# Performance work log

Measured on AMD Instinct MI355X. Metric: run time of the kernel, lower is better.

The kernel has to match this reference:

```python
import jax, jax.numpy as jnp
import numpy as np
import math

N_HEAD = 12

def _tiled_causal_mask(T):
    # t x t lower-triangular mask tiled 3x3 -> T x T (T divisible by 3)
    t = T // 3
    tril = jnp.tril(jnp.ones((t, t), dtype=bool))
    return jnp.tile(tril, (3, 3))  # [T, T]

def setup_inputs() -> dict:
    key = jax.random.key(0)
    ks = jax.random.split(key, 5)
    B, T, C = 4, 1536, 768
    s = 1.0 / math.sqrt(C)
    return {
        "x": jax.random.normal(ks[0], (B, T, C), dtype=jnp.float32),
        "Wq": jax.random.normal(ks[1], (C, C), dtype=jnp.float32) * s,
        "bq": jnp.zeros((C,), dtype=jnp.float32),
        "Wk": jax.random.normal(ks[2], (C, C), dtype=jnp.float32) * s,
        "bk": jnp.zeros((C,), dtype=jnp.float32),
        "Wv": jax.random.normal(ks[3], (C, C), dtype=jnp.float32) * s,
        "bv": jnp.zeros((C,), dtype=jnp.float32),
        "Wp": jax.random.normal(ks[4], (C, C), dtype=jnp.float32) * s,
        "bp": jnp.zeros((C,), dtype=jnp.float32),
    }

def reference(x, Wq, bq, Wk, bk, Wv, bv, Wp, bp):
    B, T, C = x.shape
    H = N_HEAD
    D = C // H  # head dim
    def heads(W, b):
        return (x @ W.T + b).reshape(B, T, H, D).transpose(0, 2, 1, 3)  # [B,H,T,D]
    q = heads(Wq, bq)
    k = heads(Wk, bk)
    v = heads(Wv, bv)
    att = jnp.einsum('bhqd,bhkd->bhqk', q, k) * (1.0 / math.sqrt(D))  # [B,H,T,T]
    mask = _tiled_causal_mask(T)  # [T,T] bool
    att = jnp.where(mask[None, None], att, jnp.float32(-jnp.inf))
    att = jax.nn.softmax(att, axis=-1)
    y = jnp.einsum('bhqk,bhkd->bhqd', att, v)  # [B,H,T,D]
    y = y.transpose(0, 2, 1, 3).reshape(B, T, C)
    return y @ Wp.T + bp
```

## Files before the change

### kernel.cpp

```cpp
#include <hip/hip_runtime.h>
#include <hip/hip_bf16.h>

typedef __attribute__((ext_vector_type(8))) short bf16x8;
typedef __attribute__((ext_vector_type(4))) float f32x4;

#define NH 12
#define HD 64
#define TT 1536
#define CC 768
#define BB 4
#define MM (BB * TT)
#define LOG2E 1.44269504088896f
#define SSHIFT 14.4269504089f

__device__ __forceinline__ unsigned short f2bf(float f) {
    unsigned int u = __builtin_bit_cast(unsigned int, f);
    return (unsigned short)((u + 0x7FFFu + ((u >> 16) & 1u)) >> 16);
}

__device__ __forceinline__ unsigned short nbf(float f) {
    __hip_bfloat16 h = __float2bfloat16(f);
    return __builtin_bit_cast(unsigned short, h);
}

__device__ __forceinline__ void gl_lds16(const unsigned short* g, unsigned short* l) {
    __builtin_amdgcn_global_load_lds(
        (const __attribute__((address_space(1))) void*)g,
        (__attribute__((address_space(3))) void*)l,
        16, 0, 0);
}

#define N4W (CC * CC / 4)
#define N4X (MM * CC / 4)
__global__ __launch_bounds__(256) void convert_all(
    const float* __restrict__ x,
    const float* __restrict__ w0, const float* __restrict__ w1,
    const float* __restrict__ w2, const float* __restrict__ w3,
    unsigned short* __restrict__ xo,
    unsigned short* __restrict__ o0, unsigned short* __restrict__ o1,
    unsigned short* __restrict__ o2, unsigned short* __restrict__ o3) {
    int i = blockIdx.x * 256 + threadIdx.x;
    const float* in;
    unsigned short* out;
    int j;
    if (i < N4X) {
        in = x; out = xo; j = i;
    } else {
        int t = i - N4X;
        int which = t / N4W;
        j = t - which * N4W;
        in = which == 0 ? w0 : which == 1 ? w1 : which == 2 ? w2 : w3;
        out = which == 0 ? o0 : which == 1 ? o1 : which == 2 ? o2 : o3;
    }
    float4 v = reinterpret_cast<const float4*>(in)[j];
    ushort4 o = { f2bf(v.x), f2bf(v.y), f2bf(v.z), f2bf(v.w) };
    reinterpret_cast<ushort4*>(out)[j] = o;
}

#define GEMM_KLOOP(APTR, BPTR)                                                \
    for (int kt = 0; kt < 12; kt++) {                                         \
        const int k0 = kt * 64;                                               \
        __syncthreads();                                                      \
        _Pragma("unroll")                                                     \
        for (int i = 0; i < 4; i++) {                                         \
            gl_lds16(&APTR[(size_t)(m0 + i * 32 + sr) * CC + k0 + sc],        \
                     as0 + (i * 32 + w * 8) * 64);                            \
            gl_lds16(&BPTR[(size_t)(n0 + i * 32 + sr) * CC + k0 + sc],        \
                     bs0 + (i * 32 + w * 8) * 64);                            \
        }                                                                     \
        __syncthreads();                                                      \
        _Pragma("unroll")                                                     \
        for (int s = 0; s < 2; s++) {                                         \
            const int swz = ((s * 4 + fg) ^ (fr & 7)) * 8;                    \
            bf16x8 a[4], b[4];                                                \
            _Pragma("unroll")                                                 \
            for (int mi = 0; mi < 4; mi++)                                    \
                a[mi] = *reinterpret_cast<const bf16x8*>(                     \
                    as0 + (wr * 64 + mi * 16 + fr) * 64 + swz);               \
            _Pragma("unroll")                                                 \
            for (int ni = 0; ni < 4; ni++)                                    \
                b[ni] = *reinterpret_cast<const bf16x8*>(                     \
                    bs0 + (wc * 64 + ni * 16 + fr) * 64 + swz);               \
            _Pragma("unroll")                                                 \
            for (int mi = 0; mi < 4; mi++)                                    \
                _Pragma("unroll")                                             \
                for (int ni = 0; ni < 4; ni++)                                \
                    acc[mi][ni] = __builtin_amdgcn_mfma_f32_16x16x32_bf16(    \
                        a[mi], b[ni], acc[mi][ni], 0, 0, 0);                  \
        }                                                                     \
    }

__global__ __launch_bounds__(256) void gemm_qkv(
    const unsigned short* __restrict__ xb,
    const unsigned short* __restrict__ wq, const float* __restrict__ bq,
    const unsigned short* __restrict__ wk, const float* __restrict__ bk,
    const unsigned short* __restrict__ wv, const float* __restrict__ bv,
    unsigned short* __restrict__ qo, unsigned short* __restrict__ ko,
    unsigned short* __restrict__ vo) {
    __shared__ unsigned short As[128][64];
    __shared__ unsigned short Bs[128][64];

    const int wg = (blockIdx.x & 7) * 108 + (blockIdx.x >> 3);
    const int z = wg / 288;
    const int rem = wg % 288;
    const int m0 = (rem / 6) * 128;
    const int n0 = (rem % 6) * 128;

    const unsigned short* W = (z == 0) ? wq : (z == 1) ? wk : wv;
    const float* bias = (z == 0) ? bq : (z == 1) ? bk : bv;
    unsigned short* out = (z == 0) ? qo : (z == 1) ? ko : vo;
    const float scale = (z == 0) ? 0.125f * LOG2E : 1.0f;

    const int tid = threadIdx.x;
    const int lane = tid & 63;
    const int w = tid >> 6;
    const int wr = w >> 1, wc = w & 1;
    const int fr = lane & 15, fg = lane >> 4;

    const int sr = tid >> 3;
    const int sc = ((tid & 7) ^ ((tid >> 3) & 7)) * 8;
    unsigned short* as0 = &As[0][0];
    unsigned short* bs0 = &Bs[0][0];

    f32x4 acc[4][4];
#pragma unroll
    for (int ni = 0; ni < 4; ni++) {
        float bv_ = bias[n0 + wc * 64 + ni * 16 + fr];
#pragma unroll
        for (int mi = 0; mi < 4; mi++)
            acc[mi][ni] = (f32x4){bv_, bv_, bv_, bv_};
    }

    GEMM_KLOOP(xb, W)

#pragma unroll
    for (int mi = 0; mi < 4; mi++)
#pragma unroll
        for (int ni = 0; ni < 4; ni++) {
            int n = n0 + wc * 64 + ni * 16 + fr;
            int h = n >> 6, d = n & 63;
            int m_base = m0 + wr * 64 + mi * 16 + fg * 4;
            int b_ = m_base / TT, t0 = m_base % TT;
            if (z == 2) {
                size_t off = ((size_t)(b_ * NH + h) * HD + d) * (size_t)TT + t0;
                ushort4 o = { nbf(acc[mi][ni][0]), nbf(acc[mi][ni][1]),
                              nbf(acc[mi][ni][2]), nbf(acc[mi][ni][3]) };
                *reinterpret_cast<ushort4*>(&out[off]) = o;
            } else {
#pragma unroll
                for (int r = 0; r < 4; r++) {
                    size_t off = ((size_t)(b_ * NH + h) * TT + t0 + r) * (size_t)HD + d;
                    out[off] = nbf(acc[mi][ni][r] * scale);
                }
            }
        }
}

__global__ __launch_bounds__(256) void gemm_proj(
    const unsigned short* __restrict__ yb,
    const unsigned short* __restrict__ wp, const float* __restrict__ bp,
    float* __restrict__ out) {
    __shared__ unsigned short As[128][64];
    __shared__ unsigned short Bs[128][64];

    const int wg = (blockIdx.x & 7) * 36 + (blockIdx.x >> 3);
    const int m0 = (wg / 6) * 128;
    const int n0 = (wg % 6) * 128;

    const int tid = threadIdx.x;
    const int lane = tid & 63;
    const int w = tid >> 6;
    const int wr = w >> 1, wc = w & 1;
    const int fr = lane & 15, fg = lane >> 4;

    const int sr = tid >> 3;
    const int sc = ((tid & 7) ^ ((tid >> 3) & 7)) * 8;
    unsigned short* as0 = &As[0][0];
    unsigned short* bs0 = &Bs[0][0];

    f32x4 acc[4][4];
#pragma unroll
    for (int ni = 0; ni < 4; ni++) {
        float bv_ = bp[n0 + wc * 64 + ni * 16 + fr];
#pragma unroll
        for (int mi = 0; mi < 4; mi++)
            acc[mi][ni] = (f32x4){bv_, bv_, bv_, bv_};
    }

    GEMM_KLOOP(yb, wp)

#pragma unroll
    for (int mi = 0; mi < 4; mi++)
#pragma unroll
        for (int ni = 0; ni < 4; ni++) {
            int n = n0 + wc * 64 + ni * 16 + fr;
#pragma unroll
            for (int r = 0; r < 4; r++) {
                int m = m0 + wr * 64 + mi * 16 + fg * 4 + r;
                out[(size_t)m * CC + n] = acc[mi][ni][r];
            }
        }
}

__global__ __launch_bounds__(256) void attn(
    const unsigned short* __restrict__ q, const unsigned short* __restrict__ k,
    const unsigned short* __restrict__ vt, unsigned short* __restrict__ y) {
    __shared__ unsigned short Ks[2][32][72];
    __shared__ unsigned short Vs[2][64][40];
    __shared__ unsigned short Ps[4][16][40];

    const int gid = blockIdx.x;
    const int slot = gid & 7;
    const int sub = (gid >> 3) % 6;
    const int bh = slot * 6 + sub;
    const int qt = gid / 48;
    const int qseg = 7 - qt / 3;
    const int sg0 = qt % 3;
    const int q0 = sg0 * 512 + qseg * 64;

    const int tid = threadIdx.x;
    const int w = tid >> 6;
    const int lane = tid & 63;
    const int fr = lane & 15, fg = lane >> 4;

    const size_t base = (size_t)bh * TT * HD;

    bf16x8 aq[2];
#pragma unroll
    for (int s = 0; s < 2; s++)
        aq[s] = *reinterpret_cast<const bf16x8*>(
            &q[base + (size_t)(q0 + w * 16 + fr) * HD + s * 32 + fg * 8]);

    f32x4 acc_o[4];
#pragma unroll
    for (int i = 0; i < 4; i++) acc_o[i] = (f32x4){0.f, 0.f, 0.f, 0.f};
    f32x4 acc_l = (f32x4){0.f, 0.f, 0.f, 0.f};

    const bf16x8 ones8 = {(short)0x3F80, (short)0x3F80, (short)0x3F80, (short)0x3F80,
                          (short)0x3F80, (short)0x3F80, (short)0x3F80, (short)0x3F80};
    const f32x4 sinit = {-SSHIFT, -SSHIFT, -SSHIFT, -SSHIFT};

    const int kr = tid >> 3, kc = tid & 7;
    const int vr = tid >> 2, vc = tid & 3;

    uint4 kreg, vreg;
    auto issue = [&](int k0n) {
        kreg = *reinterpret_cast<const uint4*>(&k[base + (size_t)(k0n + kr) * HD + kc * 8]);
        vreg = *reinterpret_cast<const uint4*>(&vt[base + (size_t)vr * TT + k0n + vc * 8]);
    };
    auto wlds = [&](int b) {
        *reinterpret_cast<uint4*>(&Ks[b][kr][kc * 8]) = kreg;
        *reinterpret_cast<uint4*>(&Vs[b][vr][vc * 8]) = vreg;
    };

    const int per = 2 * qseg + 2;
    const int ntot = 3 * per;

    issue(0);
    wlds(0);
    int cur = 0;
    int j = 0;
    int ji = 0, si = 0;

    for (int ci = 0; ci < ntot; ci++) {
        if (ci + 1 < ntot) {
            ji++; if (ji == per) { ji = 0; si++; }
            issue(si * 512 + ji * 32);
        }
        __syncthreads();

        f32x4 S[2];
#pragma unroll
        for (int nb = 0; nb < 2; nb++) {
            f32x4 sa = sinit;
#pragma unroll
            for (int s = 0; s < 2; s++) {
                bf16x8 bk_ = *reinterpret_cast<const bf16x8*>(
                    &Ks[cur][nb * 16 + fr][s * 32 + fg * 8]);
                sa = __builtin_amdgcn_mfma_f32_16x16x32_bf16(aq[s], bk_, sa, 0, 0, 0);
            }
            S[nb] = sa;
        }

        if (j >= 2 * qseg) {
            const int joff = (j - 2 * qseg) * 32;
#pragma unroll
            for (int nb = 0; nb < 2; nb++)
#pragma unroll
                for (int r = 0; r < 4; r++) {
                    int ib = w * 16 + fg * 4 + r;
                    int jb = joff + nb * 16 + fr;
                    if (jb > ib) S[nb][r] = -1e30f;
                }
        }

#pragma unroll
        for (int nb = 0; nb < 2; nb++)
#pragma unroll
            for (int r = 0; r < 4; r++)
                Ps[w][fg * 4 + r][((nb ^ (fg >> 1)) * 16) + fr] =
                    nbf(exp2f(S[nb][r]));

        bf16x8 ap = *reinterpret_cast<const bf16x8*>(
            &Ps[w][fr][(fg ^ (2 * (fr >> 3))) * 8]);
#pragma unroll
        for (int nd = 0; nd < 4; nd++) {
            bf16x8 bv_ = *reinterpret_cast<const bf16x8*>(&Vs[cur][nd * 16 + fr][fg * 8]);
            acc_o[nd] = __builtin_amdgcn_mfma_f32_16x16x32_bf16(ap, bv_, acc_o[nd], 0, 0, 0);
        }
        acc_l = __builtin_amdgcn_mfma_f32_16x16x32_bf16(ap, ones8, acc_l, 0, 0, 0);

        if (ci + 1 < ntot) wlds(cur ^ 1);
        cur ^= 1;
        if (++j == per) j = 0;
    }

    const int b_ = bh / NH, h = bh % NH;
#pragma unroll
    for (int r = 0; r < 4; r++) {
        float inv = 1.f / acc_l[r];
        int t = q0 + w * 16 + fg * 4 + r;
        size_t off = ((size_t)b_ * TT + t) * CC + h * HD;
#pragma unroll
        for (int nd = 0; nd < 4; nd++)
            y[off + nd * 16 + fr] = nbf(acc_o[nd][r] * inv);
    }
}

extern "C" void kernel_launch(void* const* d_in, const int* in_sizes, int n_in,
                              void* d_out, int out_size, void* d_ws, size_t ws_size,
                              hipStream_t stream) {
    const float* x  = (const float*)d_in[0];
    const float* Wq = (const float*)d_in[1];
    const float* bq = (const float*)d_in[2];
    const float* Wk = (const float*)d_in[3];
    const float* bk = (const float*)d_in[4];
    const float* Wv = (const float*)d_in[5];
    const float* bv = (const float*)d_in[6];
    const float* Wp = (const float*)d_in[7];
    const float* bp = (const float*)d_in[8];
    float* out = (float*)d_out;

    unsigned short* ws  = (unsigned short*)d_ws;
    unsigned short* wqb = ws;
    unsigned short* wkb = wqb + (size_t)CC * CC;
    unsigned short* wvb = wkb + (size_t)CC * CC;
    unsigned short* wpb = wvb + (size_t)CC * CC;
    unsigned short* xb  = wpb + (size_t)CC * CC;
    unsigned short* qb_ = xb  + (size_t)MM * CC;
    unsigned short* kb_ = qb_ + (size_t)MM * CC;
    unsigned short* vt_ = kb_ + (size_t)MM * CC;
    unsigned short* yb  = vt_ + (size_t)MM * CC;

    const int ntot4 = N4X + 4 * N4W;
    convert_all<<<(ntot4 + 255) / 256, 256, 0, stream>>>(
        x, Wq, Wk, Wv, Wp, xb, wqb, wkb, wvb, wpb);

    gemm_qkv<<<dim3(864), 256, 0, stream>>>(
        xb, wqb, bq, wkb, bk, wvb, bv, qb_, kb_, vt_);
    attn<<<dim3(48 * 24), 256, 0, stream>>>(qb_, kb_, vt_, yb);
    gemm_proj<<<dim3(288), 256, 0, stream>>>(yb, wpb, bp, out);
}
```

Baseline: 108.8 us.

## Shrink attention blocks to 32-row query tiles with XOR-swizzled LDS tiles

The attention kernel now runs two waves per block over 32 query rows instead of four waves over 64 rows, and launches twice as many blocks. The diagonal mask applies only to the last key tile of each segment, so fewer partially-masked tiles are processed. K and V shared-memory tiles drop their padding and use an XOR swizzle to avoid bank conflicts, with each thread loading two 16-byte chunks. The aim is finer causal load balancing, less wasted masked work, and less LDS. The cost is that each K/V tile is shared by fewer waves, so more global traffic per unit of compute.

```diff
diff --git a/kernel.cpp b/kernel.cpp
--- a/kernel.cpp
+++ b/kernel.cpp
@@ -202,21 +202,21 @@
         }
 }
 
-__global__ __launch_bounds__(256) void attn(
+__global__ __launch_bounds__(128) void attn(
     const unsigned short* __restrict__ q, const unsigned short* __restrict__ k,
     const unsigned short* __restrict__ vt, unsigned short* __restrict__ y) {
-    __shared__ unsigned short Ks[2][32][72];
-    __shared__ unsigned short Vs[2][64][40];
-    __shared__ unsigned short Ps[4][16][40];
+    __shared__ unsigned short Ks[2][32][64];
+    __shared__ unsigned short Vs[2][64][32];
+    __shared__ unsigned short Ps[2][16][40];
 
     const int gid = blockIdx.x;
     const int slot = gid & 7;
-    const int sub = (gid >> 3) % 6;
-    const int bh = slot * 6 + sub;
-    const int qt = gid / 48;
-    const int qseg = 7 - qt / 3;
-    const int sg0 = qt % 3;
-    const int q0 = sg0 * 512 + qseg * 64;
+    const int rest = gid >> 3;
+    const int bh = slot * 6 + rest % 6;
+    const int rank = rest / 6;
+    const int p32 = 15 - rank / 3;
+    const int sg0 = rank % 3;
+    const int q0 = sg0 * 512 + p32 * 32;
 
     const int tid = threadIdx.x;
     const int w = tid >> 6;
@@ -240,20 +240,26 @@
                           (short)0x3F80, (short)0x3F80, (short)0x3F80, (short)0x3F80};
     const f32x4 sinit = {-SSHIFT, -SSHIFT, -SSHIFT, -SSHIFT};
 
-    const int kr = tid >> 3, kc = tid & 7;
-    const int vr = tid >> 2, vc = tid & 3;
-
-    uint4 kreg, vreg;
+    const int kr = tid >> 2, kc0 = (tid & 3) * 2;
+    const int vr = tid >> 1, vc0 = (tid & 1) * 2;
+
+    uint4 kreg[2], vreg[2];
     auto issue = [&](int k0n) {
-        kreg = *reinterpret_cast<const uint4*>(&k[base + (size_t)(k0n + kr) * HD + kc * 8]);
-        vreg = *reinterpret_cast<const uint4*>(&vt[base + (size_t)vr * TT + k0n + vc * 8]);
+        const unsigned short* kp = &k[base + (size_t)(k0n + kr) * HD];
+        kreg[0] = *reinterpret_cast<const uint4*>(kp + ((kc0)     ^ (kr & 7)) * 8);
+        kreg[1] = *reinterpret_cast<const uint4*>(kp + ((kc0 + 1) ^ (kr & 7)) * 8);
+        const unsigned short* vp = &vt[base + (size_t)vr * TT + k0n];
+        vreg[0] = *reinterpret_cast<const uint4*>(vp + ((vc0)     ^ (vr & 3)) * 8);
+        vreg[1] = *reinterpret_cast<const uint4*>(vp + ((vc0 + 1) ^ (vr & 3)) * 8);
     };
     auto wlds = [&](int b) {
-        *reinterpret_cast<uint4*>(&Ks[b][kr][kc * 8]) = kreg;
-        *reinterpret_cast<uint4*>(&Vs[b][vr][vc * 8]) = vreg;
+        *reinterpret_cast<uint4*>(&Ks[b][kr][kc0 * 8]) = kreg[0];
+        *reinterpret_cast<uint4*>(&Ks[b][kr][kc0 * 8 + 8]) = kreg[1];
+        *reinterpret_cast<uint4*>(&Vs[b][vr][vc0 * 8]) = vreg[0];
+        *reinterpret_cast<uint4*>(&Vs[b][vr][vc0 * 8 + 8]) = vreg[1];
     };
 
-    const int per = 2 * qseg + 2;
+    const int per = p32 + 1;
     const int ntot = 3 * per;
 
     issue(0);
@@ -273,23 +279,23 @@
 #pragma unroll
         for (int nb = 0; nb < 2; nb++) {
             f32x4 sa = sinit;
+            const int krow = nb * 16 + fr;
 #pragma unroll
             for (int s = 0; s < 2; s++) {
                 bf16x8 bk_ = *reinterpret_cast<const bf16x8*>(
-                    &Ks[cur][nb * 16 + fr][s * 32 + fg * 8]);
+                    &Ks[cur][krow][(((s * 4 + fg) ^ (krow & 7))) * 8]);
                 sa = __builtin_amdgcn_mfma_f32_16x16x32_bf16(aq[s], bk_, sa, 0, 0, 0);
             }
             S[nb] = sa;
         }
 
-        if (j >= 2 * qseg) {
-            const int joff = (j - 2 * qseg) * 32;
+        if (j == per - 1) {
 #pragma unroll
             for (int nb = 0; nb < 2; nb++)
 #pragma unroll
                 for (int r = 0; r < 4; r++) {
                     int ib = w * 16 + fg * 4 + r;
-                    int jb = joff + nb * 16 + fr;
+                    int jb = nb * 16 + fr;
                     if (jb > ib) S[nb][r] = -1e30f;
                 }
         }
@@ -305,7 +311,9 @@
             &Ps[w][fr][(fg ^ (2 * (fr >> 3))) * 8]);
 #pragma unroll
         for (int nd = 0; nd < 4; nd++) {
-            bf16x8 bv_ = *reinterpret_cast<const bf16x8*>(&Vs[cur][nd * 16 + fr][fg * 8]);
+            const int vrow = nd * 16 + fr;
+            bf16x8 bv_ = *reinterpret_cast<const bf16x8*>(
+                &Vs[cur][vrow][((fg ^ (vrow & 3))) * 8]);
             acc_o[nd] = __builtin_amdgcn_mfma_f32_16x16x32_bf16(ap, bv_, acc_o[nd], 0, 0, 0);
         }
         acc_l = __builtin_amdgcn_mfma_f32_16x16x32_bf16(ap, ones8, acc_l, 0, 0, 0);
@@ -358,6 +366,6 @@
 
     gemm_qkv<<<dim3(864), 256, 0, stream>>>(
         xb, wqb, bq, wkb, bk, wvb, bv, qb_, kb_, vt_);
-    attn<<<dim3(48 * 24), 256, 0, stream>>>(qb_, kb_, vt_, yb);
+    attn<<<dim3(2304), 128, 0, stream>>>(qb_, kb_, vt_, yb);
     gemm_proj<<<dim3(288), 256, 0, stream>>>(yb, wpb, bp, out);
 }
```

New measurement: 206.5 us. 89.8% more time.
